# Kernel tuning notes

Measured on AMD Instinct MI355X. Metric: run time of the kernel, lower is better.

## Reference

```python
import jax, jax.numpy as jnp
import numpy as np

B, D, N = 8, 512, 4096
K = 2048  # codebook_size


def setup_inputs() -> dict:
    key = jax.random.key(0)
    k1, k2 = jax.random.split(key)
    x = jax.random.normal(k1, (B, D, N), dtype=jnp.float32)
    embed = jax.random.normal(k2, (K, D), dtype=jnp.float32)
    return {"x": x, "embed": embed}


def reference(x, embed):
    # x: [b, d, n] -> [b, n, d] (project_in is Identity since codebook_dim == dim)
    xt = jnp.transpose(x, (0, 2, 1))  # [b, n, d]
    # squared euclidean distances (argmin-equivalent to torch.cdist argmin)
    x2 = jnp.sum(xt * xt, axis=-1, keepdims=True)          # [b, n, 1]
    e2 = jnp.sum(embed * embed, axis=-1)                   # [k]
    cross = jnp.einsum("bnd,kd->bnk", xt, embed)           # [b, n, k]
    dist = x2 - 2.0 * cross + e2                           # [b, n, k]
    embed_ind = jnp.argmin(dist, axis=-1)                  # [b, n] int
    quantize = embed[embed_ind]                            # [b, n, d] gather
    # project_out Identity, then rearrange 'b n d -> b d n'
    quantize = jnp.transpose(quantize, (0, 2, 1))          # [b, d, n]
    return quantize, embed_ind
```

## Files before the change

kernel.cpp:

```cpp
#include <hip/hip_runtime.h>
#include <math.h>

#define DDIM 512
#define NNN  4096
#define KKK  2048
#define MMM  32768

#define TMQ  128
#define TNC  256
#define BK   32
#define KSPLIT 2
#define KHALF (KKK/KSPLIT)
#define NKT  (KHALF/TNC)
#define NDR  (DDIM/BK)
#define TOTR (NKT*NDR)
#define BUFS ((TMQ+TNC)*BK)
#define NBUF 3
#define TAU  0.05f
#define CAPF 4096

#define XH_OFF   0
#define EH_OFF   8388608
#define PART_OFF (EH_OFF + 524288)
#define XF_OFF   (PART_OFF + MMM*KSPLIT*4)
#define KEY_OFF  (XF_OFF + 2097152)
#define LIST_OFF (KEY_OFF + 8192)
#define CNT_OFF  (LIST_OFF + CAPF)
#define IDX_OFF  ((size_t)MMM * DDIM)

typedef short short8v __attribute__((ext_vector_type(8)));
typedef _Float16 half8v __attribute__((ext_vector_type(8)));
typedef float f32x4   __attribute__((ext_vector_type(4)));

__device__ inline unsigned short f2h(float f) {
  _Float16 h = (_Float16)f;
  return *(unsigned short*)&h;
}

__device__ inline void gl_lds16(const short* g, short* l) {
  __builtin_amdgcn_global_load_lds(
      (const __attribute__((address_space(1))) unsigned int*)g,
      (__attribute__((address_space(3))) unsigned int*)l, 16, 0, 0);
}

__device__ inline unsigned mono(float f) {
  unsigned u = __float_as_uint(f);
  return (u & 0x80000000u) ? ~u : (u | 0x80000000u);
}

__global__ __launch_bounds__(256)
void conv_xe(const float* __restrict__ x, const float* __restrict__ embed,
             float* __restrict__ halfe2, float* __restrict__ out) {
  __shared__ float xt[64][65];
  const int t = threadIdx.x;

  if (blockIdx.x >= 4096) {
    const int blk = blockIdx.x - 4096;
    const int gid = blk * 256 + t;
    if (gid == 0) *(int*)&out[CNT_OFF] = 0;
    if (gid < CAPF) ((unsigned long long*)&out[KEY_OFF])[gid] = ~0ull;
    const int row  = blk * 4 + (t >> 6);
    const int lane = t & 63;
    const float* e = embed + (size_t)row * DDIM;
    short* eh = (short*)&out[EH_OFF];
    const float4 v0 = *(const float4*)&e[lane*8];
    const float4 v1 = *(const float4*)&e[lane*8 + 4];
    const float vv[8] = {v0.x,v0.y,v0.z,v0.w,v1.x,v1.y,v1.z,v1.w};
    float s = 0.f;
    short8v p;
    #pragma unroll
    for (int i = 0; i < 8; ++i) { s = fmaf(vv[i], vv[i], s); p[i] = (short)f2h(vv[i]); }
    *(short8v*)&eh[(size_t)row * DDIM + lane*8] = p;
    #pragma unroll
    for (int off = 32; off >= 1; off >>= 1) s += __shfl_xor(s, off, 64);
    if (lane == 0) halfe2[row] = 0.5f * s;
    return;
  }

  const int nt = blockIdx.x & 63, dt = (blockIdx.x >> 6) & 7, b = blockIdx.x >> 9;
  const int n0 = nt * 64, d0 = dt * 64;
  const float* xb = x + ((size_t)b * DDIM + d0) * NNN + n0;
  #pragma unroll
  for (int i = 0; i < 4; ++i) {
    const int fid = t + 256*i;
    const int dl = fid >> 4, n4 = (fid & 15) * 4;
    const float4 v = *(const float4*)&xb[(size_t)dl * NNN + n4];
    xt[dl][n4+0] = v.x; xt[dl][n4+1] = v.y; xt[dl][n4+2] = v.z; xt[dl][n4+3] = v.w;
  }
  __syncthreads();
  short* xh = (short*)&out[XH_OFF];
  const int m0 = b * NNN + n0;
  #pragma unroll
  for (int i = 0; i < 2; ++i) {
    const int id = t + 256*i;
    const int m = id >> 3, ch = (id & 7) * 8;
    short8v p;
    #pragma unroll
    for (int j = 0; j < 8; ++j) p[j] = (short)f2h(xt[ch + j][m]);
    *(short8v*)&xh[(size_t)(m0 + m) * DDIM + d0 + ch] = p;
  }
}

__global__ __launch_bounds__(256, 2)
void vq_main(const float* __restrict__ halfe2, float* __restrict__ out) {
  __shared__ __align__(16) short lds[NBUF * BUFS];
  const short* xh = (const short*)&out[XH_OFF];
  const short* eh = (const short*)&out[EH_OFF];

  const int t  = threadIdx.x;
  const int mb = blockIdx.x >> 1, ks = blockIdx.x & 1;
  const int q0 = mb * TMQ;
  const int kbase = ks * KHALF;
  const int w = t >> 6, lane = t & 63;
  const int mw = (w >> 1) * 64, nw = (w & 1) * 128;
  const int l15 = lane & 15, lg = lane >> 4;
  const int c0 = w * 6;
  const int lrow = lane >> 2;
  const int scol = ((((lane & 3) - ((lane >> 3) & 3)) & 3) << 3);

  float rv1[16], rv2[16]; int ri1[16];
  #pragma unroll
  for (int i = 0; i < 16; ++i) { rv1[i] = INFINITY; rv2[i] = INFINITY; ri1[i] = 0x7FFFFFFF; }

  auto STAGE = [&](int R, int tb) {
    const int kt_ = R >> 4, dr_ = R & 15;
    const int kb_ = kbase + kt_ * TNC;
    const int d0_ = dr_ * BK;
    short* buf = lds + tb * BUFS;
    #pragma unroll
    for (int j = 0; j < 6; ++j) {
      const int c = c0 + j;
      const short* src = (c < 8)
        ? xh + (size_t)(q0 + c*16 + lrow) * DDIM + d0_ + scol
        : eh + (size_t)(kb_ + (c-8)*16 + lrow) * DDIM + d0_ + scol;
      gl_lds16(src, buf + c * 512);
    }
  };

  STAGE(0, 0);
  STAGE(1, 1);
  asm volatile("s_waitcnt vmcnt(6)" ::: "memory");
  __builtin_amdgcn_s_barrier();

  int bi = 0;
  for (int kt = 0; kt < NKT; ++kt) {
    const int kb = kbase + kt * TNC;
    f32x4 acc[4][8];
    #pragma unroll
    for (int mi = 0; mi < 4; ++mi)
      #pragma unroll
      for (int ni = 0; ni < 8; ++ni) acc[mi][ni] = (f32x4){0.f,0.f,0.f,0.f};

    for (int dr = 0; dr < NDR; ++dr) {
      const int R = kt * NDR + dr;
      const int nb = bi ? bi - 1 : 2;
      if (R + 2 < TOTR) STAGE(R + 2, nb);
      const short* xs = lds + bi * BUFS;
      const short* es = xs + TMQ * BK;
      half8v bfr[8];
      #pragma unroll
      for (int ni = 0; ni < 8; ++ni) {
        const int row = nw + ni*16 + l15;
        bfr[ni] = *(const half8v*)&es[row*32 + (((lg + (row >> 1)) & 3) << 3)];
      }
      #pragma unroll
      for (int mi = 0; mi < 4; ++mi) {
        const int row = mw + mi*16 + l15;
        const half8v a = *(const half8v*)&xs[row*32 + (((lg + (row >> 1)) & 3) << 3)];
        #pragma unroll
        for (int ni = 0; ni < 8; ++ni)
          acc[mi][ni] = __builtin_amdgcn_mfma_f32_16x16x32_f16(a, bfr[ni], acc[mi][ni], 0,0,0);
      }
      if (R + 2 < TOTR) { asm volatile("s_waitcnt vmcnt(6)" ::: "memory"); }
      else              { asm volatile("s_waitcnt vmcnt(0)" ::: "memory"); }
      __builtin_amdgcn_s_barrier();
      bi = (bi == 2) ? 0 : bi + 1;
    }

    float he[8];
    #pragma unroll
    for (int ni = 0; ni < 8; ++ni) he[ni] = halfe2[kb + nw + ni*16 + l15];
    #pragma unroll
    for (int mi = 0; mi < 4; ++mi) {
      #pragma unroll
      for (int r = 0; r < 4; ++r) {
        const int e_ = mi*4 + r;
        #pragma unroll
        for (int ni = 0; ni < 8; ++ni) {
          const float sc = he[ni] - acc[mi][ni][r];
          if (sc < rv1[e_]) { rv2[e_] = rv1[e_]; rv1[e_] = sc; ri1[e_] = kb + nw + ni*16 + l15; }
          else rv2[e_] = fminf(rv2[e_], sc);
        }
      }
    }
  }

  #pragma unroll
  for (int e_ = 0; e_ < 16; ++e_) {
    float v1 = rv1[e_], v2 = rv2[e_]; int i1 = ri1[e_];
    #pragma unroll
    for (int off = 1; off < 16; off <<= 1) {
      const float ov1 = __shfl_xor(v1, off, 64);
      const int   oi1 = __shfl_xor(i1, off, 64);
      const float ov2 = __shfl_xor(v2, off, 64);
      if (ov1 < v1 || (ov1 == v1 && oi1 < i1)) { v2 = fminf(v1, ov2); v1 = ov1; i1 = oi1; }
      else v2 = fminf(v2, ov1);
    }
    rv1[e_] = v1; rv2[e_] = v2; ri1[e_] = i1;
  }

  __syncthreads();
  float* mbuf = (float*)lds;
  if (l15 == 0) {
    #pragma unroll
    for (int mi = 0; mi < 4; ++mi)
      #pragma unroll
      for (int r = 0; r < 4; ++r) {
        const int ql = mw + mi*16 + lg*4 + r;
        const int slot = (ql*2 + (w & 1))*3;
        const int e_ = mi*4 + r;
        mbuf[slot+0] = rv1[e_];
        mbuf[slot+1] = __int_as_float(ri1[e_]);
        mbuf[slot+2] = rv2[e_];
      }
  }
  __syncthreads();
  if (t < TMQ) {
    const float a1 = mbuf[t*6+0]; const int ai = __float_as_int(mbuf[t*6+1]); const float a2 = mbuf[t*6+2];
    const float b1 = mbuf[t*6+3]; const int bi2 = __float_as_int(mbuf[t*6+4]); const float b2 = mbuf[t*6+5];
    float v1, v2; int i1;
    if (b1 < a1 || (b1 == a1 && bi2 < ai)) { v1 = b1; i1 = bi2; v2 = fminf(a1, b2); }
    else                                   { v1 = a1; i1 = ai;  v2 = fminf(a2, b1); }
    f32x4 st = {v1, (float)i1, v2, 0.f};
    *(f32x4*)&out[PART_OFF + ((size_t)(q0 + t)*KSPLIT + ks)*4] = st;
  }
}

__global__ void vq_merge(float* __restrict__ out) {
  const int q = blockIdx.x * 256 + threadIdx.x;
  float v1, v2; int i1;
  {
    const f32x4 p = *(const f32x4*)&out[PART_OFF + (size_t)q*(KSPLIT*4)];
    v1 = p[0]; i1 = (int)p[1]; v2 = p[2];
  }
  #pragma unroll
  for (int s = 1; s < KSPLIT; ++s) {
    const f32x4 p = *(const f32x4*)&out[PART_OFF + (size_t)q*(KSPLIT*4) + s*4];
    const float b1 = p[0]; const int bi = (int)p[1]; const float b2 = p[2];
    if (b1 < v1 || (b1 == v1 && bi < i1)) { v2 = fminf(v1, b2); v1 = b1; i1 = bi; }
    else v2 = fminf(v2, b1);
  }
  out[IDX_OFF + q] = (float)i1;
  if (v2 - v1 < TAU) {
    const int pos = atomicAdd((int*)&out[CNT_OFF], 1);
    if (pos < CAPF) ((int*)&out[LIST_OFF])[pos] = q;
  }
}

__global__ __launch_bounds__(256)
void vq_prep(const float* __restrict__ x, float* __restrict__ out) {
  const int nf0 = *(const int*)&out[CNT_OFF];
  const int nf  = nf0 < CAPF ? nf0 : CAPF;
  const int* list = (const int*)&out[LIST_OFF];
  float* XF = &out[XF_OFF];
  const int wid  = (blockIdx.x * 256 + threadIdx.x) >> 6;
  const int lane = threadIdx.x & 63;
  for (int s = wid; s < nf; s += 1024) {
    const int q = list[s];
    const int b = q >> 12, n = q & (NNN - 1);
    const float* xb = x + (size_t)b * DDIM * NNN + n;
    #pragma unroll
    for (int j = 0; j < 8; ++j) {
      const int d = lane + 64*j;
      XF[(size_t)s * DDIM + d] = xb[(size_t)d * NNN];
    }
  }
}

__global__ __launch_bounds__(256, 2)
void vq_refine(const float* __restrict__ embed, const float* __restrict__ halfe2,
               float* __restrict__ out) {
  const int nf0 = *(const int*)&out[CNT_OFF];
  const int nf  = nf0 < CAPF ? nf0 : CAPF;
  const int s0  = blockIdx.y * 64;
  if (s0 >= nf) return;
  __shared__ float xs[32][68];
  __shared__ float es[32][132];
  const int t = threadIdx.x, tx = t & 15, ty = t >> 4;
  const int kb = blockIdx.x * 128;
  const float* XF = &out[XF_OFF];
  unsigned long long* keys = (unsigned long long*)&out[KEY_OFF];

  float acc[4][8];
  #pragma unroll
  for (int i = 0; i < 4; ++i)
    #pragma unroll
    for (int j = 0; j < 8; ++j) acc[i][j] = 0.f;

  for (int dc = 0; dc < 16; ++dc) {
    __syncthreads();
    #pragma unroll
    for (int i = 0; i < 2; ++i) {
      const int l = t + 256*i;
      const int m = l >> 3, f = l & 7;
      const float4 v = *(const float4*)&XF[(size_t)(s0 + m) * DDIM + dc*32 + 4*f];
      xs[4*f+0][m] = v.x; xs[4*f+1][m] = v.y; xs[4*f+2][m] = v.z; xs[4*f+3][m] = v.w;
    }
    #pragma unroll
    for (int i = 0; i < 4; ++i) {
      const int l = t + 256*i;
      const int k = l >> 3, f = l & 7;
      const float4 v = *(const float4*)&embed[(size_t)(kb + k)*DDIM + dc*32 + 4*f];
      es[4*f+0][k] = v.x; es[4*f+1][k] = v.y; es[4*f+2][k] = v.z; es[4*f+3][k] = v.w;
    }
    __syncthreads();
    #pragma unroll
    for (int d = 0; d < 32; ++d) {
      const float4 a4 = *(const float4*)&xs[d][ty*4];
      const float4 b0 = *(const float4*)&es[d][tx*4];
      const float4 b1 = *(const float4*)&es[d][64 + tx*4];
      const float a[4]  = {a4.x, a4.y, a4.z, a4.w};
      const float bb[8] = {b0.x, b0.y, b0.z, b0.w, b1.x, b1.y, b1.z, b1.w};
      #pragma unroll
      for (int i = 0; i < 4; ++i)
        #pragma unroll
        for (int j = 0; j < 8; ++j)
          acc[i][j] = fmaf(a[i], bb[j], acc[i][j]);
    }
  }

  const int kb0 = kb + tx*4, kb1 = kb + 64 + tx*4;
  const float4 h0 = *(const float4*)&halfe2[kb0];
  const float4 h1 = *(const float4*)&halfe2[kb1];
  const float hh[8] = {h0.x, h0.y, h0.z, h0.w, h1.x, h1.y, h1.z, h1.w};
  #pragma unroll
  for (int i = 0; i < 4; ++i) {
    float v = hh[0] - acc[i][0];
    int  vi = kb0;
    #pragma unroll
    for (int j = 1; j < 8; ++j) {
      const float w  = hh[j] - acc[i][j];
      const int   wk = (j < 4) ? (kb0 + j) : (kb1 + j - 4);
      if (w < v) { v = w; vi = wk; }
    }
    #pragma unroll
    for (int off = 1; off < 16; off <<= 1) {
      const float ov = __shfl_xor(v, off, 64);
      const int   oi = __shfl_xor(vi, off, 64);
      if (ov < v || (ov == v && oi < vi)) { v = ov; vi = oi; }
    }
    if (tx == 0) {
      const unsigned long long key =
          ((unsigned long long)mono(v) << 32) | (unsigned)vi;
      atomicMin(&keys[s0 + ty*4 + i], key);
    }
  }
}

__global__ void vq_apply(float* __restrict__ out) {
  const int slot = blockIdx.x * 256 + threadIdx.x;
  const int nf0 = *(const int*)&out[CNT_OFF];
  const int nf  = nf0 < CAPF ? nf0 : CAPF;
  if (slot >= nf) return;
  const int q = ((const int*)&out[LIST_OFF])[slot];
  const unsigned long long k = ((const unsigned long long*)&out[KEY_OFF])[slot];
  if (k != ~0ull) out[IDX_OFF + q] = (float)(unsigned)(k & 0xFFFFFFFFull);
}

__global__ __launch_bounds__(256)
void vq_gather(const float* __restrict__ embed, float* __restrict__ out) {
  __shared__ int idx_s[128];
  const int t  = threadIdx.x;
  const int q0 = blockIdx.x * 128;
  const int b  = q0 >> 12, n0 = q0 & (NNN-1);
  if (t < 128) idx_s[t] = (int)out[IDX_OFF + q0 + t];
  __syncthreads();
  float* qb = out + (size_t)b * DDIM * NNN + n0;
  for (int j = 0; j < 64; ++j) {
    const int id = t + 256*j;
    const int d = id >> 5, n4 = (id & 31) * 4;
    float4 v;
    v.x = embed[(size_t)idx_s[n4+0]*DDIM + d];
    v.y = embed[(size_t)idx_s[n4+1]*DDIM + d];
    v.z = embed[(size_t)idx_s[n4+2]*DDIM + d];
    v.w = embed[(size_t)idx_s[n4+3]*DDIM + d];
    *(float4*)&qb[(size_t)d * NNN + n4] = v;
  }
}

extern "C" void kernel_launch(void* const* d_in, const int* in_sizes, int n_in,
                              void* d_out, int out_size, void* d_ws, size_t ws_size,
                              hipStream_t stream) {
  const float* x     = (const float*)d_in[0];
  const float* embed = (const float*)d_in[1];
  float* out    = (float*)d_out;
  float* halfe2 = (float*)d_ws;

  hipLaunchKernelGGL(conv_xe, dim3(4096 + KKK/4), dim3(256), 0, stream, x, embed, halfe2, out);
  hipLaunchKernelGGL(vq_main,  dim3((MMM/TMQ)*KSPLIT), dim3(256), 0, stream, halfe2, out);
  hipLaunchKernelGGL(vq_merge, dim3(MMM/256), dim3(256), 0, stream, out);
  hipLaunchKernelGGL(vq_prep,  dim3(256),     dim3(256), 0, stream, x, out);
  hipLaunchKernelGGL(vq_refine,dim3(16, CAPF/64), dim3(256), 0, stream, embed, halfe2, out);
  hipLaunchKernelGGL(vq_apply, dim3(CAPF/256),dim3(256), 0, stream, out);
  hipLaunchKernelGGL(vq_gather,dim3(MMM/128), dim3(256), 0, stream, embed, out);
}
```

Baseline: 302.1 us.

## Fuse refine-candidate prep into merge and stage gathered rows in LDS

The separate vq_prep kernel is removed. Its job of copying flagged query columns of x into the refine buffer now runs inside vq_merge: each wavefront uses a ballot over flagged lanes and shuffles to copy each column, which saves a launch and a read of the list. vq_gather now loads the 32 selected codebook rows per block into shared memory with coalesced float4 reads, then writes the transposed output from LDS instead of doing scattered strided global reads. The trade-offs are more LDS per block (about 66KB, limiting occupancy) and serialized per-wave copy loops inside merge.

```diff
diff --git a/kernel.cpp b/kernel.cpp
--- a/kernel.cpp
+++ b/kernel.cpp
@@ -236,7 +236,7 @@
   }
 }
 
-__global__ void vq_merge(float* __restrict__ out) {
+__global__ void vq_merge(const float* __restrict__ x, float* __restrict__ out) {
   const int q = blockIdx.x * 256 + threadIdx.x;
   float v1, v2; int i1;
   {
@@ -251,28 +251,26 @@
     else v2 = fminf(v2, b1);
   }
   out[IDX_OFF + q] = (float)i1;
+  int pos = -1;
   if (v2 - v1 < TAU) {
-    const int pos = atomicAdd((int*)&out[CNT_OFF], 1);
+    pos = atomicAdd((int*)&out[CNT_OFF], 1);
     if (pos < CAPF) ((int*)&out[LIST_OFF])[pos] = q;
-  }
-}
-
-__global__ __launch_bounds__(256)
-void vq_prep(const float* __restrict__ x, float* __restrict__ out) {
-  const int nf0 = *(const int*)&out[CNT_OFF];
-  const int nf  = nf0 < CAPF ? nf0 : CAPF;
-  const int* list = (const int*)&out[LIST_OFF];
+    else pos = -1;
+  }
+  unsigned long long mask = __ballot(pos >= 0);
+  const int lane = threadIdx.x & 63;
   float* XF = &out[XF_OFF];
-  const int wid  = (blockIdx.x * 256 + threadIdx.x) >> 6;
-  const int lane = threadIdx.x & 63;
-  for (int s = wid; s < nf; s += 1024) {
-    const int q = list[s];
-    const int b = q >> 12, n = q & (NNN - 1);
-    const float* xb = x + (size_t)b * DDIM * NNN + n;
+  while (mask) {
+    const int src = __ffsll(mask) - 1;
+    mask &= mask - 1;
+    const int qq = __shfl(q,   src, 64);
+    const int pp = __shfl(pos, src, 64);
+    const int bb = qq >> 12, nn = qq & (NNN - 1);
+    const float* xb = x + (size_t)bb * DDIM * NNN + nn;
     #pragma unroll
     for (int j = 0; j < 8; ++j) {
       const int d = lane + 64*j;
-      XF[(size_t)s * DDIM + d] = xb[(size_t)d * NNN];
+      XF[(size_t)pp * DDIM + d] = xb[(size_t)d * NNN];
     }
   }
 }
@@ -369,21 +367,31 @@
 
 __global__ __launch_bounds__(256)
 void vq_gather(const float* __restrict__ embed, float* __restrict__ out) {
-  __shared__ int idx_s[128];
+  __shared__ float ls[32][516];
+  __shared__ int idx_s[32];
   const int t  = threadIdx.x;
-  const int q0 = blockIdx.x * 128;
+  const int q0 = blockIdx.x * 32;
   const int b  = q0 >> 12, n0 = q0 & (NNN-1);
-  if (t < 128) idx_s[t] = (int)out[IDX_OFF + q0 + t];
+  if (t < 32) idx_s[t] = (int)out[IDX_OFF + q0 + t];
+  __syncthreads();
+  {
+    const int rh  = t >> 7;
+    const int col = (t & 127) * 4;
+    #pragma unroll
+    for (int p = 0; p < 16; ++p) {
+      const int r = p*2 + rh;
+      const float4 v = *(const float4*)&embed[(size_t)idx_s[r]*DDIM + col];
+      *(float4*)&ls[r][col] = v;
+    }
+  }
   __syncthreads();
   float* qb = out + (size_t)b * DDIM * NNN + n0;
-  for (int j = 0; j < 64; ++j) {
-    const int id = t + 256*j;
-    const int d = id >> 5, n4 = (id & 31) * 4;
+  #pragma unroll
+  for (int j = 0; j < 16; ++j) {
+    const int d  = 32*j + (t >> 3);
+    const int n4 = (t & 7) * 4;
     float4 v;
-    v.x = embed[(size_t)idx_s[n4+0]*DDIM + d];
-    v.y = embed[(size_t)idx_s[n4+1]*DDIM + d];
-    v.z = embed[(size_t)idx_s[n4+2]*DDIM + d];
-    v.w = embed[(size_t)idx_s[n4+3]*DDIM + d];
+    v.x = ls[n4+0][d]; v.y = ls[n4+1][d]; v.z = ls[n4+2][d]; v.w = ls[n4+3][d];
     *(float4*)&qb[(size_t)d * NNN + n4] = v;
   }
 }
@@ -398,9 +406,8 @@
 
   hipLaunchKernelGGL(conv_xe, dim3(4096 + KKK/4), dim3(256), 0, stream, x, embed, halfe2, out);
   hipLaunchKernelGGL(vq_main,  dim3((MMM/TMQ)*KSPLIT), dim3(256), 0, stream, halfe2, out);
-  hipLaunchKernelGGL(vq_merge, dim3(MMM/256), dim3(256), 0, stream, out);
-  hipLaunchKernelGGL(vq_prep,  dim3(256),     dim3(256), 0, stream, x, out);
+  hipLaunchKernelGGL(vq_merge, dim3(MMM/256), dim3(256), 0, stream, x, out);
   hipLaunchKernelGGL(vq_refine,dim3(16, CAPF/64), dim3(256), 0, stream, embed, halfe2, out);
   hipLaunchKernelGGL(vq_apply, dim3(CAPF/256),dim3(256), 0, stream, out);
-  hipLaunchKernelGGL(vq_gather,dim3(MMM/128), dim3(256), 0, stream, embed, out);
-}
+  hipLaunchKernelGGL(vq_gather,dim3(MMM/32),  dim3(256), 0, stream, embed, out);
+}
```

Result: faster. 267.1 us (-11.6%).
